# Performance work log

Measured on AMD Instinct MI355X. Metric: run time of the kernel, lower is better.

## Reference

```python
import jax, jax.numpy as jnp
import numpy as np

IN_DIM = 32
OUT_DIM = 32
VAR_DIM = 64
BATCH = 16384
KER_DIMS = [1024, 1024, 1024, 1024]
NUM_STEPS = 8  # fixed-step RK4 stand-in for adaptive odeint (tol=1e-4)


def setup_inputs() -> dict:
    key = jax.random.key(0)
    ks = jax.random.split(key, 12)
    x = jax.random.normal(ks[0], (BATCH, IN_DIM), dtype=jnp.float32)
    aug = jnp.ones((BATCH, VAR_DIM - IN_DIM), dtype=jnp.float32)
    dims = [VAR_DIM] + KER_DIMS + [VAR_DIM]
    inp = {"x": x, "aug": aug}
    for i, (d1, d2) in enumerate(zip(dims[:-1], dims[1:])):
        # Linear(d1+1, d2): weight (d2, d1+1), bias (d2,)
        inp[f"W{i}"] = jax.random.normal(ks[1 + 2 * i], (d2, d1 + 1), dtype=jnp.float32) * 0.02
        inp[f"b{i}"] = jax.random.normal(ks[2 + 2 * i], (d2,), dtype=jnp.float32) * 0.02
    return inp


def _odefunc(t, y, Ws, bs):
    # y: [B, VAR_DIM]; per-layer concat of scalar time column, Linear, ReLU (except last)
    out = y
    n = len(Ws)
    for i, (W, b) in enumerate(zip(Ws, bs)):
        z = jnp.concatenate([out, jnp.full((out.shape[0], 1), t, dtype=out.dtype)], axis=1)
        out = z @ W.T + b
        if i < n - 1:
            out = jax.nn.relu(out)
    return out


def _integrate(y0, Ws, bs):
    dt = jnp.float32(1.0 / NUM_STEPS)

    def rk4_step(y, t):
        k1 = _odefunc(t, y, Ws, bs)
        k2 = _odefunc(t + 0.5 * dt, y + 0.5 * dt * k1, Ws, bs)
        k3 = _odefunc(t + 0.5 * dt, y + 0.5 * dt * k2, Ws, bs)
        k4 = _odefunc(t + dt, y + dt * k3, Ws, bs)
        return y + (dt / 6.0) * (k1 + 2.0 * k2 + 2.0 * k3 + k4), None

    ts = jnp.arange(NUM_STEPS, dtype=jnp.float32) * dt
    y1, _ = jax.lax.scan(rk4_step, y0, ts)
    return y1


def reference(x, aug, W0, b0, W1, b1, W2, b2, W3, b3, W4, b4):
    Ws = (W0, W1, W2, W3, W4)
    bs = (b0, b1, b2, b3, b4)
    y0 = jnp.concatenate([x, aug], axis=1)  # [B, VAR_DIM]
    y1 = _integrate(y0, Ws, bs)
    return y1[:, :OUT_DIM]
```

## Files before the change

### kernel.cpp

```cpp
#include <hip/hip_runtime.h>
#include <cstdint>
#include <cstddef>

#define BATCH 16384

typedef float f32x4 __attribute__((ext_vector_type(4)));
typedef _Float16 f16x8 __attribute__((ext_vector_type(8)));

__device__ __forceinline__ unsigned short f2h_bits(float f) {
  _Float16 h = (_Float16)f;
  return __builtin_bit_cast(unsigned short, h);
}

__device__ __forceinline__ void async_cp16(const void* g, void* l) {
  __builtin_amdgcn_global_load_lds(
      (const __attribute__((address_space(1))) unsigned int*)g,
      (__attribute__((address_space(3))) unsigned int*)l, 16, 0, 0);
}

#define PIPE_BAR_3() asm volatile("s_waitcnt vmcnt(3)\n\ts_barrier" ::: "memory")
#define PIPE_BAR_0() asm volatile("s_waitcnt vmcnt(0)\n\ts_barrier" ::: "memory")

template <int BM, int BN, int RT, int CT, int K, int N, bool RELU>
__launch_bounds__(512, 4)
__global__ void gemm_h(const unsigned short* __restrict__ A,
                       const unsigned short* __restrict__ Bw,
                       const float* __restrict__ Wfull,
                       const float* __restrict__ bias,
                       float tval,
                       unsigned short* __restrict__ Ch) {
  constexpr int BK = 32;
  constexpr int NI = K / BK;
  static_assert(NI >= 2, "pipeline needs >=2 stages");
  static_assert((BM * 4 + BN * 4) / 512 == 3, "vmcnt(3) assumes 3 loads/stage");
  static_assert(BM == 4 * RT * 16 && BN == 2 * CT * 16, "4x2 waves");
  __shared__ __align__(16) unsigned short smA[3][BM * BK];
  __shared__ __align__(16) unsigned short smB[3][BN * BK];
  __shared__ float biasLds[BN];

  const int tid = threadIdx.x;
  const int wave = tid >> 6;
  const int lane = tid & 63;
  const int quad = lane >> 4;
  const int r16 = lane & 15;

  const int rowA0 = blockIdx.x * BM;
  const int rowB0 = blockIdx.y * BN;
  const int waveM = wave >> 1;
  const int waveN = wave & 1;

  if (tid < BN) {
    const int col = rowB0 + tid;
    biasLds[tid] = bias[col] + tval * Wfull[(size_t)col * (K + 1) + K];
  }

  auto stage = [&](int k0, int buf) {
#pragma unroll
    for (int i = 0; i < BM * 4 / 512; ++i) {
      const int s = i * 512 + tid;
      const int row = s >> 2;
      const int c = (s & 3) ^ ((row >> 1) & 3);
      const unsigned short* g = A + (size_t)(rowA0 + row) * K + (k0 + c * 8);
      char* l = ((char*)smA[buf]) + (size_t)(i * 512 + (wave << 6)) * 16;
      async_cp16(g, l);
    }
    {
      const int s = tid;
      const int row = s >> 2;
      const int c = (s & 3) ^ ((row >> 1) & 3);
      const unsigned short* g = Bw + (size_t)(rowB0 + row) * K + (k0 + c * 8);
      char* l = ((char*)smB[buf]) + (size_t)((wave << 6)) * 16;
      async_cp16(g, l);
    }
  };

  f32x4 acc[RT][CT];
  const f32x4 zero = {0.f, 0.f, 0.f, 0.f};
#pragma unroll
  for (int i = 0; i < RT; ++i)
#pragma unroll
    for (int j = 0; j < CT; ++j) acc[i][j] = zero;

  auto compute = [&](int buf) {
    const unsigned short* sA = smA[buf];
    const unsigned short* sB = smB[buf];
    f16x8 af[RT], bfr[CT];
#pragma unroll
    for (int nt = 0; nt < CT; ++nt) {
      const int row = waveN * (CT * 16) + nt * 16 + r16;
      const int cp = quad ^ ((row >> 1) & 3);
      bfr[nt] = *(const f16x8*)(sB + row * BK + cp * 8);
    }
#pragma unroll
    for (int mt = 0; mt < RT; ++mt) {
      const int row = waveM * (RT * 16) + mt * 16 + r16;
      const int cp = quad ^ ((row >> 1) & 3);
      af[mt] = *(const f16x8*)(sA + row * BK + cp * 8);
    }
#pragma unroll
    for (int mt = 0; mt < RT; ++mt)
#pragma unroll
      for (int nt = 0; nt < CT; ++nt)
        acc[mt][nt] =
            __builtin_amdgcn_mfma_f32_16x16x32_f16(af[mt], bfr[nt], acc[mt][nt], 0, 0, 0);
  };

  stage(0, 0);
  stage(BK, 1);

#pragma unroll
  for (int kk = 0; kk < NI - 1; ++kk) {
    PIPE_BAR_3();
    if (kk + 2 < NI) stage((kk + 2) * BK, (kk + 2) % 3);
    compute(kk % 3);
  }
  PIPE_BAR_0();
  compute((NI - 1) % 3);

#pragma unroll
  for (int mt = 0; mt < RT; ++mt) {
    const int grow0 = rowA0 + waveM * (RT * 16) + mt * 16 + quad * 4;
#pragma unroll
    for (int nt = 0; nt < CT; ++nt) {
      const int lcol = waveN * (CT * 16) + nt * 16 + r16;
      const int gcol = rowB0 + lcol;
      const float bi = biasLds[lcol];
#pragma unroll
      for (int r = 0; r < 4; ++r) {
        float v = acc[mt][nt][r] + bi;
        if (RELU) v = fmaxf(v, 0.0f);
        Ch[(size_t)(grow0 + r) * N + gcol] = f2h_bits(v);
      }
    }
  }
}

#define SBAR  asm volatile("s_barrier" ::: "memory")
#define VBAR4 asm volatile("s_waitcnt vmcnt(4)\n\ts_barrier" ::: "memory")
#define VBAR0 asm volatile("s_waitcnt vmcnt(0)\n\ts_barrier" ::: "memory")

#define PHASE(sA_, sB_, Q, STAGE_STMT, BND)                                   \
  {                                                                           \
    if ((Q) == 0) {                                                           \
      _Pragma("unroll") for (int nt = 0; nt < 4; ++nt) {                      \
        const int row = wc * 64 + nt * 16 + r16;                              \
        const int sw = row & 7;                                               \
        const unsigned short* bp = (sB_) + row * 64;                          \
        bfr[nt][0] = *(const f16x8*)(bp + ((quad ^ sw) << 3));                \
        bfr[nt][1] = *(const f16x8*)(bp + (((4 + quad) ^ sw) << 3));          \
      }                                                                       \
    }                                                                         \
    f16x8 af0[2], af1[2];                                                     \
    _Pragma("unroll") for (int mi = 0; mi < 2; ++mi) {                        \
      const int row = wr * 128 + ((Q) * 2 + mi) * 16 + r16;                   \
      const int sw = row & 7;                                                 \
      const unsigned short* ap = (sA_) + row * 64;                            \
      af0[mi] = *(const f16x8*)(ap + ((quad ^ sw) << 3));                     \
      af1[mi] = *(const f16x8*)(ap + (((4 + quad) ^ sw) << 3));               \
    }                                                                         \
    STAGE_STMT;                                                               \
    if ((Q) == 0) asm volatile("s_waitcnt lgkmcnt(8)" ::: "memory");          \
    SBAR;                                                                     \
    __builtin_amdgcn_s_setprio(1);                                            \
    _Pragma("unroll") for (int mi = 0; mi < 2; ++mi)                          \
      _Pragma("unroll") for (int nt = 0; nt < 4; ++nt) {                      \
        acc[(Q) * 2 + mi][nt] = __builtin_amdgcn_mfma_f32_16x16x32_f16(       \
            af0[mi], bfr[nt][0], acc[(Q) * 2 + mi][nt], 0, 0, 0);             \
        acc[(Q) * 2 + mi][nt] = __builtin_amdgcn_mfma_f32_16x16x32_f16(       \
            af1[mi], bfr[nt][1], acc[(Q) * 2 + mi][nt], 0, 0, 0);             \
      }                                                                       \
    __builtin_amdgcn_s_setprio(0);                                            \
    BND;                                                                      \
  }

#define TILE(sA_, sB_, S0, S1, S2, S3, BND)    \
  {                                            \
    f16x8 bfr[4][2];                           \
    PHASE(sA_, sB_, 0, S0, SBAR)               \
    PHASE(sA_, sB_, 1, S1, SBAR)               \
    PHASE(sA_, sB_, 2, S2, SBAR)               \
    PHASE(sA_, sB_, 3, S3, BND)                \
  }

__launch_bounds__(512, 2)
__global__ void gemm8(const unsigned short* __restrict__ A,
                      const unsigned short* __restrict__ Bw,
                      const float* __restrict__ Wfull,
                      const float* __restrict__ bias,
                      float tval,
                      unsigned short* __restrict__ Ch) {
  __shared__ __align__(16) unsigned short smA[2][256 * 64];
  __shared__ __align__(16) unsigned short smB[2][256 * 64];
  __shared__ float biasLds[256];

  const int tid = threadIdx.x;
  const int wave = tid >> 6;
  const int lane = tid & 63;
  const int quad = lane >> 4;
  const int r16 = lane & 15;
  const int wr = wave >> 2;
  const int wc = wave & 3;

  const int orig = blockIdx.y * gridDim.x + blockIdx.x;
  const int swz = (orig & 7) * 32 + (orig >> 3);
  const int tx = swz & 63;
  const int ty = swz >> 6;

  const int rowA0 = tx * 256;
  const int rowB0 = ty * 256;
  const unsigned short* Ag = A + (size_t)rowA0 * 1024;
  const unsigned short* Bg = Bw + (size_t)rowB0 * 1024;

  if (tid < 256) {
    const int col = rowB0 + tid;
    biasLds[tid] = bias[col] + tval * Wfull[(size_t)col * 1025 + 1024];
  }

  auto stg = [&](const unsigned short* gbase, unsigned short* lds, int k0, int half) {
#pragma unroll
    for (int i = 0; i < 2; ++i) {
      const int s = half * 1024 + i * 512 + tid;
      const int row = s >> 3;
      const int c = (s & 7) ^ (row & 7);
      const unsigned short* g = gbase + (size_t)row * 1024 + (k0 + (c << 3));
      char* l = (char*)lds + (size_t)(half * 1024 + i * 512 + (wave << 6)) * 16;
      async_cp16(g, l);
    }
  };

  f32x4 acc[8][4];
  const f32x4 zero = {0.f, 0.f, 0.f, 0.f};
#pragma unroll
  for (int i = 0; i < 8; ++i)
#pragma unroll
    for (int j = 0; j < 4; ++j) acc[i][j] = zero;

  stg(Ag, smA[0], 0, 0);  stg(Ag, smA[0], 0, 1);
  stg(Bg, smB[0], 0, 0);  stg(Bg, smB[0], 0, 1);
  stg(Bg, smB[1], 64, 0); stg(Bg, smB[1], 64, 1);
  VBAR4;

  for (int tt = 0; tt < 14; tt += 2) {
    const int ka0 = (tt + 1) * 64;
    const int kb0 = (tt + 2) * 64;
    TILE(smA[0], smB[0],
         stg(Ag, smA[1], ka0, 0),
         stg(Ag, smA[1], ka0, 1),
         stg(Bg, smB[0], kb0, 0),
         stg(Bg, smB[0], kb0, 1),
         VBAR4)
    const int ka1 = (tt + 2) * 64;
    const int kb1 = (tt + 3) * 64;
    TILE(smA[1], smB[1],
         stg(Ag, smA[0], ka1, 0),
         stg(Ag, smA[0], ka1, 1),
         stg(Bg, smB[1], kb1, 0),
         stg(Bg, smB[1], kb1, 1),
         VBAR4)
  }
  TILE(smA[0], smB[0],
       stg(Ag, smA[1], 15 * 64, 0),
       stg(Ag, smA[1], 15 * 64, 1),
       ;, ;, VBAR0)
  TILE(smA[1], smB[1], ;, ;, ;, ;, ;)

#pragma unroll
  for (int mt = 0; mt < 8; ++mt) {
    const int grow0 = rowA0 + wr * 128 + mt * 16 + quad * 4;
#pragma unroll
    for (int nt = 0; nt < 4; ++nt) {
      const int lcol = wc * 64 + nt * 16 + r16;
      const int gcol = rowB0 + lcol;
      const float bi = biasLds[lcol];
#pragma unroll
      for (int r = 0; r < 4; ++r) {
        float v = acc[mt][nt][r] + bi;
        v = fmaxf(v, 0.0f);
        Ch[(size_t)(grow0 + r) * 1024 + gcol] = f2h_bits(v);
      }
    }
  }
}

__launch_bounds__(256, 4)
__global__ void gemm_l4(const unsigned short* __restrict__ A,
                        const unsigned short* __restrict__ Bw,
                        const float* __restrict__ Wfull,
                        const float* __restrict__ bias,
                        float tval,
                        float* __restrict__ y, float* __restrict__ ksum,
                        unsigned short* __restrict__ yh,
                        float* __restrict__ outp, int mode, float dt) {
  constexpr int K = 1024, BK = 32, BM = 32, BN = 64, NI = K / BK;
  __shared__ __align__(16) unsigned short smA[2][BM * BK];
  __shared__ __align__(16) unsigned short smB[2][BN * BK];
  __shared__ float biasLds[BN];

  const int tid = threadIdx.x;
  const int wave = tid >> 6;
  const int lane = tid & 63;
  const int quad = lane >> 4;
  const int r16 = lane & 15;

  const int rowA0 = blockIdx.x * BM;
  const int waveM = wave >> 1;
  const int waveN = wave & 1;

  if (tid < BN) {
    biasLds[tid] = bias[tid] + tval * Wfull[(size_t)tid * (K + 1) + K];
  }

  auto stage = [&](int k0, int buf) {
    if (tid < BM * 4) {
      const int s = tid;
      const int row = s >> 2;
      const int c = (s & 3) ^ ((row >> 1) & 3);
      const unsigned short* g = A + (size_t)(rowA0 + row) * K + (k0 + c * 8);
      char* l = ((char*)smA[buf]) + (size_t)(wave << 6) * 16;
      async_cp16(g, l);
    }
    {
      const int s = tid;
      const int row = s >> 2;
      const int c = (s & 3) ^ ((row >> 1) & 3);
      const unsigned short* g = Bw + (size_t)row * K + (k0 + c * 8);
      char* l = ((char*)smB[buf]) + (size_t)(wave << 6) * 16;
      async_cp16(g, l);
    }
  };

  f32x4 acc[2];
  const f32x4 zero = {0.f, 0.f, 0.f, 0.f};
  acc[0] = zero; acc[1] = zero;

  stage(0, 0);

#pragma unroll 2
  for (int kk = 0; kk < NI; ++kk) {
    __syncthreads();
    if (kk + 1 < NI) stage((kk + 1) * BK, (kk + 1) & 1);

    const unsigned short* sA = smA[kk & 1];
    const unsigned short* sB = smB[kk & 1];
    f16x8 af, bfr[2];
    {
      const int row = waveM * 16 + r16;
      const int cp = quad ^ ((row >> 1) & 3);
      af = *(const f16x8*)(sA + row * BK + cp * 8);
    }
#pragma unroll
    for (int nt = 0; nt < 2; ++nt) {
      const int row = (waveN * 2 + nt) * 16 + r16;
      const int cp = quad ^ ((row >> 1) & 3);
      bfr[nt] = *(const f16x8*)(sB + row * BK + cp * 8);
    }
#pragma unroll
    for (int nt = 0; nt < 2; ++nt)
      acc[nt] = __builtin_amdgcn_mfma_f32_16x16x32_f16(af, bfr[nt], acc[nt], 0, 0, 0);
  }

  const int grow0 = rowA0 + waveM * 16 + quad * 4;
#pragma unroll
  for (int nt = 0; nt < 2; ++nt) {
    const int col = waveN * 32 + nt * 16 + r16;
    const float bi = biasLds[col];
#pragma unroll
    for (int r = 0; r < 4; ++r) {
      const float k = acc[nt][r] + bi;
      const int row = grow0 + r;
      const int idx = row * 64 + col;
      if (mode == 0) {
        ksum[idx] = k;
        yh[idx] = f2h_bits(y[idx] + 0.5f * dt * k);
      } else if (mode == 1) {
        ksum[idx] += 2.f * k;
        yh[idx] = f2h_bits(y[idx] + 0.5f * dt * k);
      } else if (mode == 2) {
        ksum[idx] += 2.f * k;
        yh[idx] = f2h_bits(y[idx] + dt * k);
      } else {
        const float yn = y[idx] + (dt / 6.f) * (ksum[idx] + k);
        y[idx] = yn;
        yh[idx] = f2h_bits(yn);
        if (outp && col < 32) outp[row * 32 + col] = yn;
      }
    }
  }
}

__global__ void conv_w(const float* __restrict__ W, unsigned short* __restrict__ Wh,
                       int N, int K) {
  const int idx = blockIdx.x * 256 + threadIdx.x;
  if (idx < N * K) {
    const int n = idx / K;
    const int k = idx - n * K;
    Wh[idx] = f2h_bits(W[(size_t)n * (K + 1) + k]);
  }
}

__global__ void init_y(const float* __restrict__ x, const float* __restrict__ aug,
                       float* __restrict__ y, unsigned short* __restrict__ yh) {
  const int idx = blockIdx.x * 256 + threadIdx.x;
  const int i = idx >> 6;
  const int j = idx & 63;
  const float v = (j < 32) ? x[i * 32 + j] : aug[i * 32 + (j - 32)];
  y[idx] = v;
  yh[idx] = f2h_bits(v);
}

extern "C" void kernel_launch(void* const* d_in, const int* in_sizes, int n_in,
                              void* d_out, int out_size, void* d_ws, size_t ws_size,
                              hipStream_t stream) {
  const float* x = (const float*)d_in[0];
  const float* aug = (const float*)d_in[1];
  const float* W[5];
  const float* b[5];
  for (int i = 0; i < 5; ++i) {
    W[i] = (const float*)d_in[2 + 2 * i];
    b[i] = (const float*)d_in[3 + 2 * i];
  }

  char* ws = (char*)d_ws;
  auto alloc = [&](size_t bytes) -> char* {
    char* p = ws;
    ws += (bytes + 255) & ~(size_t)255;
    return p;
  };
  float* y = (float*)alloc((size_t)BATCH * 64 * 4);
  unsigned short* yh = (unsigned short*)alloc((size_t)BATCH * 64 * 2);
  unsigned short* h1 = (unsigned short*)alloc((size_t)BATCH * 1024 * 2);
  unsigned short* h2 = (unsigned short*)alloc((size_t)BATCH * 1024 * 2);
  float* ksum = (float*)alloc((size_t)BATCH * 64 * 4);
  const int Kdim[5] = {64, 1024, 1024, 1024, 1024};
  const int Ndim[5] = {1024, 1024, 1024, 1024, 64};
  unsigned short* Wh[5];
  for (int i = 0; i < 5; ++i)
    Wh[i] = (unsigned short*)alloc((size_t)Ndim[i] * Kdim[i] * 2);

  for (int i = 0; i < 5; ++i) {
    const int total = Ndim[i] * Kdim[i];
    conv_w<<<(total + 255) / 256, 256, 0, stream>>>(W[i], Wh[i], Ndim[i], Kdim[i]);
  }
  init_y<<<BATCH * 64 / 256, 256, 0, stream>>>(x, aug, y, yh);

  const float dt = 0.125f;
  float* outp = (float*)d_out;

  auto eval = [&](float t, int mode, float* op) {
    gemm_h<256, 128, 4, 4, 64, 1024, true>
        <<<dim3(BATCH / 256, 1024 / 128), 512, 0, stream>>>(
            yh, Wh[0], W[0], b[0], t, h1);
    unsigned short* src = h1;
    unsigned short* dst = h2;
    for (int L = 1; L <= 3; ++L) {
      gemm8<<<dim3(BATCH / 256, 1024 / 256), 512, 0, stream>>>(
          src, Wh[L], W[L], b[L], t, dst);
      unsigned short* tmp = src; src = dst; dst = tmp;
    }
    gemm_l4<<<dim3(BATCH / 32, 1), 256, 0, stream>>>(
        src, Wh[4], W[4], b[4], t, y, ksum, yh, op, mode, dt);
  };

  for (int s = 0; s < 8; ++s) {
    const float t0 = s * dt;
    eval(t0, 0, nullptr);
    eval(t0 + 0.5f * dt, 1, nullptr);
    eval(t0 + 0.5f * dt, 2, nullptr);
    eval(t0 + dt, 3, (s == 7) ? outp : nullptr);
  }
}
```

Before: 5.113 ms.

## Split A staging by row quarters and wait on finer vmcnt per phase

A-tile staging now loads rows by phase-pair quarters (rows needed for phases 0-1 first, then 2-3), so the barrier after phase 1 only waits on the first half of the next A tile. The previous whole-tile vmcnt(4) barrier becomes vmcnt(8) after phase 1 and vmcnt(6) after phase 3, letting compute begin earlier while loads are still in flight. The block-index swizzle used for L2 locality is also removed in favor of plain blockIdx mapping. This risks worse cache reuse, and any miscounted waitcnt would read stale LDS data.

```diff
diff --git a/kernel.cpp b/kernel.cpp
--- a/kernel.cpp
+++ b/kernel.cpp
@@ -136,7 +136,8 @@
 }
 
 #define SBAR  asm volatile("s_barrier" ::: "memory")
-#define VBAR4 asm volatile("s_waitcnt vmcnt(4)\n\ts_barrier" ::: "memory")
+#define VBAR8 asm volatile("s_waitcnt vmcnt(8)\n\ts_barrier" ::: "memory")
+#define VBAR6 asm volatile("s_waitcnt vmcnt(6)\n\ts_barrier" ::: "memory")
 #define VBAR0 asm volatile("s_waitcnt vmcnt(0)\n\ts_barrier" ::: "memory")
 
 #define PHASE(sA_, sB_, Q, STAGE_STMT, BND)                                   \
@@ -173,13 +174,13 @@
     BND;                                                                      \
   }
 
-#define TILE(sA_, sB_, S0, S1, S2, S3, BND)    \
+#define TILE(sA_, sB_, S0, S1, S2, S3, B1, B3) \
   {                                            \
     f16x8 bfr[4][2];                           \
     PHASE(sA_, sB_, 0, S0, SBAR)               \
-    PHASE(sA_, sB_, 1, S1, SBAR)               \
+    PHASE(sA_, sB_, 1, S1, B1)                 \
     PHASE(sA_, sB_, 2, S2, SBAR)               \
-    PHASE(sA_, sB_, 3, S3, BND)                \
+    PHASE(sA_, sB_, 3, S3, B3)                 \
   }
 
 __launch_bounds__(512, 2)
@@ -201,13 +202,8 @@
   const int wr = wave >> 2;
   const int wc = wave & 3;
 
-  const int orig = blockIdx.y * gridDim.x + blockIdx.x;
-  const int swz = (orig & 7) * 32 + (orig >> 3);
-  const int tx = swz & 63;
-  const int ty = swz >> 6;
-
-  const int rowA0 = tx * 256;
-  const int rowB0 = ty * 256;
+  const int rowA0 = blockIdx.x * 256;
+  const int rowB0 = blockIdx.y * 256;
   const unsigned short* Ag = A + (size_t)rowA0 * 1024;
   const unsigned short* Bg = Bw + (size_t)rowB0 * 1024;
 
@@ -216,14 +212,29 @@
     biasLds[tid] = bias[col] + tval * Wfull[(size_t)col * 1025 + 1024];
   }
 
-  auto stg = [&](const unsigned short* gbase, unsigned short* lds, int k0, int half) {
+  auto stgB = [&](unsigned short* lds, int k0, int half) {
 #pragma unroll
     for (int i = 0; i < 2; ++i) {
       const int s = half * 1024 + i * 512 + tid;
       const int row = s >> 3;
       const int c = (s & 7) ^ (row & 7);
-      const unsigned short* g = gbase + (size_t)row * 1024 + (k0 + (c << 3));
+      const unsigned short* g = Bg + (size_t)row * 1024 + (k0 + (c << 3));
       char* l = (char*)lds + (size_t)(half * 1024 + i * 512 + (wave << 6)) * 16;
+      async_cp16(g, l);
+    }
+  };
+
+  auto stgA = [&](unsigned short* lds, int k0, int qp) {
+#pragma unroll
+    for (int i = 0; i < 2; ++i) {
+      const int s = i * 512 + tid;
+      const int r = s >> 3;
+      const int row = qp * 64 + (r & 63) + ((r >> 6) << 7);
+      const int c = (s & 7) ^ (row & 7);
+      const unsigned short* g = Ag + (size_t)row * 1024 + (k0 + (c << 3));
+      const int rb = i * 64 + (wave << 3);
+      const int rowb = qp * 64 + (rb & 63) + ((rb >> 6) << 7);
+      char* l = (char*)lds + (size_t)rowb * 128;
       async_cp16(g, l);
     }
   };
@@ -235,34 +246,36 @@
 #pragma unroll
     for (int j = 0; j < 4; ++j) acc[i][j] = zero;
 
-  stg(Ag, smA[0], 0, 0);  stg(Ag, smA[0], 0, 1);
-  stg(Bg, smB[0], 0, 0);  stg(Bg, smB[0], 0, 1);
-  stg(Bg, smB[1], 64, 0); stg(Bg, smB[1], 64, 1);
-  VBAR4;
+  stgA(smA[0], 0, 0);
+  stgB(smB[0], 0, 0); stgB(smB[0], 0, 1);
+  stgA(smA[0], 0, 1);
+  stgB(smB[1], 64, 0); stgB(smB[1], 64, 1);
+  VBAR6;
 
   for (int tt = 0; tt < 14; tt += 2) {
     const int ka0 = (tt + 1) * 64;
     const int kb0 = (tt + 2) * 64;
     TILE(smA[0], smB[0],
-         stg(Ag, smA[1], ka0, 0),
-         stg(Ag, smA[1], ka0, 1),
-         stg(Bg, smB[0], kb0, 0),
-         stg(Bg, smB[0], kb0, 1),
-         VBAR4)
+         stgA(smA[1], ka0, 0),
+         stgA(smA[1], ka0, 1),
+         stgB(smB[0], kb0, 0),
+         stgB(smB[0], kb0, 1),
+         VBAR8, VBAR6)
     const int ka1 = (tt + 2) * 64;
     const int kb1 = (tt + 3) * 64;
     TILE(smA[1], smB[1],
-         stg(Ag, smA[0], ka1, 0),
-         stg(Ag, smA[0], ka1, 1),
-         stg(Bg, smB[1], kb1, 0),
-         stg(Bg, smB[1], kb1, 1),
-         VBAR4)
+         stgA(smA[0], ka1, 0),
+         stgA(smA[0], ka1, 1),
+         stgB(smB[1], kb1, 0),
+         stgB(smB[1], kb1, 1),
+         VBAR8, VBAR6)
   }
   TILE(smA[0], smB[0],
-       stg(Ag, smA[1], 15 * 64, 0),
-       stg(Ag, smA[1], 15 * 64, 1),
-       ;, ;, VBAR0)
-  TILE(smA[1], smB[1], ;, ;, ;, ;, ;)
+       stgA(smA[1], 15 * 64, 0),
+       stgA(smA[1], 15 * 64, 1),
+       ;, ;,
+       VBAR8, VBAR0)
+  TILE(smA[1], smB[1], ;, ;, ;, ;, SBAR, ;)
 
 #pragma unroll
   for (int mt = 0; mt < 8; ++mt) {
```

New measurement: 4.599 ms. 10.0% less time.
